# Kernel tuning notes

Hardware: AMD Instinct MI355X
Metric: run time of the kernel (lower is better)

## Reference

```python
import jax, jax.numpy as jnp
import numpy as np


def setup_inputs() -> dict:
    key = jax.random.key(0)
    x = jax.random.normal(key, (64, 512, 16, 16), dtype=jnp.float32)
    return {"x": x}


def reference(x):
    # x: [B, dim, h, w] -> covariance pooling y: [B, dim, dim]
    B, dim, h, w = x.shape
    M = h * w
    xf = x.reshape(B, dim, M)
    # I_hat = (1/M) I - (1/M^2) 11^T  (centering matrix scaled by 1/M)
    inv_M = jnp.asarray(1.0 / M, dtype=x.dtype)
    I_hat = inv_M * jnp.eye(M, dtype=x.dtype) - (inv_M * inv_M) * jnp.ones((M, M), dtype=x.dtype)
    # y = x @ I_hat @ x^T, I_hat broadcast over batch
    xI = jnp.einsum('bdm,mn->bdn', xf, I_hat)   # [B, dim, M]
    y = jnp.einsum('bdn,ben->bde', xI, xf)      # [B, dim, dim]
    return y
```

## Files before the change

kernel.cpp:

```cpp
#include <hip/hip_runtime.h>
#include <stdint.h>


typedef __attribute__((ext_vector_type(8))) short bf16x8;
typedef __attribute__((ext_vector_type(4))) float f32x4;

static __device__ __forceinline__ unsigned short f2bf(float f) {
    union { float f; uint32_t u; } c; c.f = f;
    uint32_t u = c.u;
    return (unsigned short)((u + 0x7FFFu + ((u >> 16) & 1u)) >> 16);
}

__global__ __launch_bounds__(256) void covpool_fused(const float* __restrict__ x,
                                                     float* __restrict__ y) {
    __shared__ __align__(16) unsigned short As[128 * 32];
    __shared__ __align__(16) unsigned short Bs[128 * 32];
    __shared__ __align__(16) float muA[128];
    __shared__ __align__(16) float muB[128];

    const int xcd  = blockIdx.x & 7;
    const int j    = blockIdx.x >> 3;
    const int b    = xcd * 8 + (j >> 4);
    const int tile = j & 15;
    const int tm = tile >> 2, tn = tile & 3;
    const bool diag = (tm == tn);

    const float* Ag = x + ((size_t)b * 512 + tm * 128) * 256;
    const float* Bg = x + ((size_t)b * 512 + tn * 128) * 256;

    const int tid  = threadIdx.x;
    const int lane = tid & 63;
    const int wave = tid >> 6;
    const int wm = (wave >> 1) * 64;
    const int wn = (wave & 1) * 64;

    f32x4 acc[4][4] = {};
    float pA[2] = {0.f, 0.f}, pB[2] = {0.f, 0.f};

    const int rl  = lane & 15;
    const int swl = ((lane >> 4) ^ ((rl >> 1) & 3)) * 8;
    const int srow   = tid >> 2;
    const int schunk = tid & 3;

    for (int kk = 0; kk < 256; kk += 32) {
        __syncthreads();
#pragma unroll
        for (int t = 0; t < 2; ++t) {
            const int row  = t * 64 + srow;
            const int slot = schunk ^ ((row >> 1) & 3);
            {
                const float* g = Ag + (size_t)row * 256 + kk + schunk * 8;
                f32x4 v0 = *(const f32x4*)g;
                f32x4 v1 = *(const f32x4*)(g + 4);
                v0 *= 0.0625f; v1 *= 0.0625f;
                pA[t] += (v0.x + v0.y + v0.z + v0.w) + (v1.x + v1.y + v1.z + v1.w);
                bf16x8 o;
                o[0] = (short)f2bf(v0.x); o[1] = (short)f2bf(v0.y);
                o[2] = (short)f2bf(v0.z); o[3] = (short)f2bf(v0.w);
                o[4] = (short)f2bf(v1.x); o[5] = (short)f2bf(v1.y);
                o[6] = (short)f2bf(v1.z); o[7] = (short)f2bf(v1.w);
                *(bf16x8*)(As + row * 32 + slot * 8) = o;
            }
            if (!diag) {
                const float* g = Bg + (size_t)row * 256 + kk + schunk * 8;
                f32x4 v0 = *(const f32x4*)g;
                f32x4 v1 = *(const f32x4*)(g + 4);
                v0 *= 0.0625f; v1 *= 0.0625f;
                pB[t] += (v0.x + v0.y + v0.z + v0.w) + (v1.x + v1.y + v1.z + v1.w);
                bf16x8 o;
                o[0] = (short)f2bf(v0.x); o[1] = (short)f2bf(v0.y);
                o[2] = (short)f2bf(v0.z); o[3] = (short)f2bf(v0.w);
                o[4] = (short)f2bf(v1.x); o[5] = (short)f2bf(v1.y);
                o[6] = (short)f2bf(v1.z); o[7] = (short)f2bf(v1.w);
                *(bf16x8*)(Bs + row * 32 + slot * 8) = o;
            }
        }
        __syncthreads();

        const unsigned short* Bsrc = diag ? As : Bs;
        bf16x8 af[4], bfr[4];
#pragma unroll
        for (int i = 0; i < 4; ++i)
            af[i] = *(const bf16x8*)(As + (wm + i * 16 + rl) * 32 + swl);
#pragma unroll
        for (int jj = 0; jj < 4; ++jj)
            bfr[jj] = *(const bf16x8*)(Bsrc + (wn + jj * 16 + rl) * 32 + swl);
#pragma unroll
        for (int i = 0; i < 4; ++i)
#pragma unroll
            for (int jj = 0; jj < 4; ++jj)
                acc[i][jj] = __builtin_amdgcn_mfma_f32_16x16x32_bf16(
                    af[i], bfr[jj], acc[i][jj], 0, 0, 0);
    }

#pragma unroll
    for (int t = 0; t < 2; ++t) {
        float s = pA[t];
        s += __shfl_xor(s, 1, 64); s += __shfl_xor(s, 2, 64);
        if ((tid & 3) == 0) muA[t * 64 + srow] = s * 0.0625f;
        if (!diag) {
            float sb = pB[t];
            sb += __shfl_xor(sb, 1, 64); sb += __shfl_xor(sb, 2, 64);
            if ((tid & 3) == 0) muB[t * 64 + srow] = sb * 0.0625f;
        }
    }
    __syncthreads();

    const float* muBp = diag ? muA : muB;
    float* ybase = y + (size_t)b * 512 * 512;
    const int rowb = tm * 128 + wm + (lane >> 4) * 4;
    const int colb = tn * 128 + wn + rl;
    float cB[4];
#pragma unroll
    for (int jj = 0; jj < 4; ++jj) cB[jj] = muBp[wn + jj * 16 + rl];
#pragma unroll
    for (int i = 0; i < 4; ++i) {
        const f32x4 ma = *(const f32x4*)&muA[wm + i * 16 + (lane >> 4) * 4];
#pragma unroll
        for (int jj = 0; jj < 4; ++jj) {
            const int col = colb + jj * 16;
            const int r0  = rowb + i * 16;
#pragma unroll
            for (int r = 0; r < 4; ++r)
                ybase[(size_t)(r0 + r) * 512 + col] = acc[i][jj][r] - ma[r] * cB[jj];
        }
    }
}

extern "C" void kernel_launch(void* const* d_in, const int* in_sizes, int n_in,
                              void* d_out, int out_size, void* d_ws, size_t ws_size,
                              hipStream_t stream) {
    const float* x = (const float*)d_in[0];
    float* yout = (float*)d_out;
    (void)d_ws; (void)ws_size;
    covpool_fused<<<1024, 256, 0, stream>>>(x, yout);
}
```

Baseline: 110.5 us.

## Compute only upper-triangular tiles, mirror via LDS transpose, prefetch next K slab

Uses the symmetry of the covariance output to launch only the 10 upper-triangular 128x128 tiles per batch instead of 16, writing each off-diagonal tile twice (direct and transposed) through an LDS staging buffer. The epilogue now emits coalesced 16-byte stores instead of scattered scalar stores. Global loads for the next K slab are issued into registers before the MFMA loop of the current slab, overlapping memory latency with compute. This adds LDS usage and extra syncs in the epilogue, and the transposed read path may hit LDS bank conflicts.

New measurement: 101.8 us. 1.09x faster.

```diff
diff --git a/kernel.cpp b/kernel.cpp
--- a/kernel.cpp
+++ b/kernel.cpp
@@ -11,18 +11,32 @@
     return (unsigned short)((u + 0x7FFFu + ((u >> 16) & 1u)) >> 16);
 }
 
+static __device__ __forceinline__ void cvt_store(f32x4 v0, f32x4 v1, float* psum,
+                                                 unsigned short* dst) {
+    v0 *= 0.0625f; v1 *= 0.0625f;
+    *psum += (v0.x + v0.y + v0.z + v0.w) + (v1.x + v1.y + v1.z + v1.w);
+    bf16x8 o;
+    o[0] = (short)f2bf(v0.x); o[1] = (short)f2bf(v0.y);
+    o[2] = (short)f2bf(v0.z); o[3] = (short)f2bf(v0.w);
+    o[4] = (short)f2bf(v1.x); o[5] = (short)f2bf(v1.y);
+    o[6] = (short)f2bf(v1.z); o[7] = (short)f2bf(v1.w);
+    *(bf16x8*)dst = o;
+}
+
 __global__ __launch_bounds__(256) void covpool_fused(const float* __restrict__ x,
                                                      float* __restrict__ y) {
     __shared__ __align__(16) unsigned short As[128 * 32];
     __shared__ __align__(16) unsigned short Bs[128 * 32];
-    __shared__ __align__(16) float muA[128];
-    __shared__ __align__(16) float muB[128];
+    __shared__ __align__(16) float Ep[32 * 132];
+    __shared__ float muA[128];
+    __shared__ float muB[128];
 
-    const int xcd  = blockIdx.x & 7;
-    const int j    = blockIdx.x >> 3;
-    const int b    = xcd * 8 + (j >> 4);
-    const int tile = j & 15;
-    const int tm = tile >> 2, tn = tile & 3;
+    const int xcd = blockIdx.x & 7;
+    const int j   = blockIdx.x >> 3;
+    const int b   = xcd * 8 + j / 10;
+    const int t10 = j % 10;
+    const unsigned code = (unsigned)((0xFBA7653210ULL >> (4 * t10)) & 15ULL);
+    const int tm = code >> 2, tn = code & 3;
     const bool diag = (tm == tn);
 
     const float* Ag = x + ((size_t)b * 512 + tm * 128) * 256;
@@ -38,9 +52,20 @@
     float pA[2] = {0.f, 0.f}, pB[2] = {0.f, 0.f};
 
     const int rl  = lane & 15;
-    const int swl = ((lane >> 4) ^ ((rl >> 1) & 3)) * 8;
-    const int srow   = tid >> 2;
-    const int schunk = tid & 3;
+    const int q   = lane >> 4;
+    const int swl = (q ^ ((rl >> 1) & 3)) * 8;
+    const int srow = tid >> 2, schunk = tid & 3;
+
+    f32x4 a0[2], a1[2], b0[2], b1[2];
+#pragma unroll
+    for (int t = 0; t < 2; ++t) {
+        const float* g = Ag + (size_t)(t * 64 + srow) * 256 + schunk * 8;
+        a0[t] = *(const f32x4*)g; a1[t] = *(const f32x4*)(g + 4);
+        if (!diag) {
+            const float* h = Bg + (size_t)(t * 64 + srow) * 256 + schunk * 8;
+            b0[t] = *(const f32x4*)h; b1[t] = *(const f32x4*)(h + 4);
+        }
+    }
 
     for (int kk = 0; kk < 256; kk += 32) {
         __syncthreads();
@@ -48,35 +73,21 @@
         for (int t = 0; t < 2; ++t) {
             const int row  = t * 64 + srow;
             const int slot = schunk ^ ((row >> 1) & 3);
-            {
-                const float* g = Ag + (size_t)row * 256 + kk + schunk * 8;
-                f32x4 v0 = *(const f32x4*)g;
-                f32x4 v1 = *(const f32x4*)(g + 4);
-                v0 *= 0.0625f; v1 *= 0.0625f;
-                pA[t] += (v0.x + v0.y + v0.z + v0.w) + (v1.x + v1.y + v1.z + v1.w);
-                bf16x8 o;
-                o[0] = (short)f2bf(v0.x); o[1] = (short)f2bf(v0.y);
-                o[2] = (short)f2bf(v0.z); o[3] = (short)f2bf(v0.w);
-                o[4] = (short)f2bf(v1.x); o[5] = (short)f2bf(v1.y);
-                o[6] = (short)f2bf(v1.z); o[7] = (short)f2bf(v1.w);
-                *(bf16x8*)(As + row * 32 + slot * 8) = o;
-            }
-            if (!diag) {
-                const float* g = Bg + (size_t)row * 256 + kk + schunk * 8;
-                f32x4 v0 = *(const f32x4*)g;
-                f32x4 v1 = *(const f32x4*)(g + 4);
-                v0 *= 0.0625f; v1 *= 0.0625f;
-                pB[t] += (v0.x + v0.y + v0.z + v0.w) + (v1.x + v1.y + v1.z + v1.w);
-                bf16x8 o;
-                o[0] = (short)f2bf(v0.x); o[1] = (short)f2bf(v0.y);
-                o[2] = (short)f2bf(v0.z); o[3] = (short)f2bf(v0.w);
-                o[4] = (short)f2bf(v1.x); o[5] = (short)f2bf(v1.y);
-                o[6] = (short)f2bf(v1.z); o[7] = (short)f2bf(v1.w);
-                *(bf16x8*)(Bs + row * 32 + slot * 8) = o;
+            cvt_store(a0[t], a1[t], &pA[t], As + row * 32 + slot * 8);
+            if (!diag) cvt_store(b0[t], b1[t], &pB[t], Bs + row * 32 + slot * 8);
+        }
+        __syncthreads();
+        if (kk < 224) {
+#pragma unroll
+            for (int t = 0; t < 2; ++t) {
+                const float* g = Ag + (size_t)(t * 64 + srow) * 256 + (kk + 32) + schunk * 8;
+                a0[t] = *(const f32x4*)g; a1[t] = *(const f32x4*)(g + 4);
+                if (!diag) {
+                    const float* h = Bg + (size_t)(t * 64 + srow) * 256 + (kk + 32) + schunk * 8;
+                    b0[t] = *(const f32x4*)h; b1[t] = *(const f32x4*)(h + 4);
+                }
             }
         }
-        __syncthreads();
-
         const unsigned short* Bsrc = diag ? As : Bs;
         bf16x8 af[4], bfr[4];
 #pragma unroll
@@ -97,32 +108,55 @@
     for (int t = 0; t < 2; ++t) {
         float s = pA[t];
         s += __shfl_xor(s, 1, 64); s += __shfl_xor(s, 2, 64);
-        if ((tid & 3) == 0) muA[t * 64 + srow] = s * 0.0625f;
+        if (schunk == 0) muA[t * 64 + srow] = s * 0.0625f;
         if (!diag) {
             float sb = pB[t];
             sb += __shfl_xor(sb, 1, 64); sb += __shfl_xor(sb, 2, 64);
-            if ((tid & 3) == 0) muB[t * 64 + srow] = sb * 0.0625f;
+            if (schunk == 0) muB[t * 64 + srow] = sb * 0.0625f;
         }
     }
-    __syncthreads();
+    const float* muBp = diag ? muA : muB;
+    float* yb = y + (size_t)b * 512 * 512;
 
-    const float* muBp = diag ? muA : muB;
-    float* ybase = y + (size_t)b * 512 * 512;
-    const int rowb = tm * 128 + wm + (lane >> 4) * 4;
-    const int colb = tn * 128 + wn + rl;
-    float cB[4];
 #pragma unroll
-    for (int jj = 0; jj < 4; ++jj) cB[jj] = muBp[wn + jj * 16 + rl];
+    for (int c = 0; c < 4; ++c) {
+        __syncthreads();
+        if ((wave >> 1) == (c >> 1)) {
+            const int ii0 = 2 * (c & 1);
 #pragma unroll
-    for (int i = 0; i < 4; ++i) {
-        const f32x4 ma = *(const f32x4*)&muA[wm + i * 16 + (lane >> 4) * 4];
+            for (int ii = 0; ii < 2; ++ii) {
+                const int i = ii0 + ii;
 #pragma unroll
-        for (int jj = 0; jj < 4; ++jj) {
-            const int col = colb + jj * 16;
-            const int r0  = rowb + i * 16;
+                for (int jj = 0; jj < 4; ++jj) {
+                    const int col = wn + jj * 16 + rl;
+                    const float mb = muBp[col];
 #pragma unroll
-            for (int r = 0; r < 4; ++r)
-                ybase[(size_t)(r0 + r) * 512 + col] = acc[i][jj][r] - ma[r] * cB[jj];
+                    for (int r = 0; r < 4; ++r) {
+                        const int row = wm + i * 16 + q * 4 + r;
+                        Ep[(ii * 16 + q * 4 + r) * 132 + col] = acc[i][jj][r] - muA[row] * mb;
+                    }
+                }
+            }
+        }
+        __syncthreads();
+#pragma unroll
+        for (int v = 0; v < 4; ++v) {
+            const int flat = v * 256 + tid;
+            const int rloc = flat >> 5, c4 = flat & 31;
+            f32x4 val = *(const f32x4*)(Ep + rloc * 132 + c4 * 4);
+            *(f32x4*)(yb + (size_t)(tm * 128 + c * 32 + rloc) * 512 + tn * 128 + c4 * 4) = val;
+        }
+        if (!diag) {
+#pragma unroll
+            for (int v = 0; v < 4; ++v) {
+                const int id = v * 256 + tid;
+                const int cc = id >> 3, g = id & 7;
+                f32x4 val;
+#pragma unroll
+                for (int e = 0; e < 4; ++e)
+                    val[e] = Ep[(g * 4 + e) * 132 + cc];
+                *(f32x4*)(yb + (size_t)(tn * 128 + cc) * 512 + tm * 128 + c * 32 + g * 4) = val;
+            }
         }
     }
 }
@@ -133,5 +167,5 @@
     const float* x = (const float*)d_in[0];
     float* yout = (float*)d_out;
     (void)d_ws; (void)ws_size;
-    covpool_fused<<<1024, 256, 0, stream>>>(x, yout);
+    covpool_fused<<<640, 256, 0, stream>>>(x, yout);
 }
```
